# Kernel tuning notes

Measured on AMD Instinct MI355X. Metric: run time of the kernel, lower is better.

The kernel has to match this reference:

```python
import jax, jax.numpy as jnp
import numpy as np

H = 128      # hidden_dim
N = 200000   # number of available (job, machine) ops
M = 1000     # machine nodes
J = 5000     # job nodes


def setup_inputs() -> dict:
    key = jax.random.key(0)
    ks = jax.random.split(key, 8)
    s = 0.05  # weight scale
    return {
        "x_graph": jax.random.normal(ks[0], (1, 2 * H), jnp.float32),
        "x_m": jax.random.normal(ks[1], (M, H), jnp.float32),
        "x_job": jax.random.normal(ks[2], (J, H), jnp.float32),
        "m_ids": jax.random.randint(ks[3], (N,), 0, M),
        "job_idx": jax.random.randint(ks[4], (N,), 0, J),
        "W0": jax.random.normal(ks[5], (4 * H, H), jnp.float32) * s,
        "b0": jnp.zeros((H,), jnp.float32),
        "W1": jax.random.normal(ks[6], (H, H), jnp.float32) * s,
        "b1": jnp.zeros((H,), jnp.float32),
        "W2": jax.random.normal(ks[7], (H, 1), jnp.float32) * s,
        "b2": jnp.zeros((1,), jnp.float32),
    }


def reference(x_graph, x_m, x_job, m_ids, job_idx, W0, b0, W1, b1, W2, b2):
    n = m_ids.shape[0]
    # vectorized form of the python loop: [x_graph | x_m[m_id] | x_job[job_pos]] -> [N, 4H]
    feats = jnp.concatenate(
        [
            jnp.broadcast_to(x_graph, (n, x_graph.shape[1])),
            x_m[m_ids],
            x_job[job_idx],
        ],
        axis=1,
    )
    h = jax.nn.relu(feats @ W0 + b0)   # Linear(4H -> H) + ReLU
    h = jax.nn.relu(h @ W1 + b1)       # Linear(H -> H) + ReLU
    scores = (h @ W2 + b2)[:, 0]       # Linear(H -> 1), squeeze -> [N]
    logp = jax.nn.log_softmax(scores, axis=0)
    probs = jnp.exp(logp)
    idx = jnp.argmax(scores)           # greedy selection (deterministic baseline)
    entropy = -jnp.sum(probs * logp)   # Categorical entropy
    return idx, probs[idx], logp[idx], entropy
```

## Files before the change

kernel.cpp:

```cpp
#include <hip/hip_runtime.h>
#include <math.h>

#define HID 128
#define TILE_R 64
#define TILE_P 32
#define XS_STRIDE 132
#define H0S_STRIDE 136
#define DELTA 0.05f

typedef short bf16x8 __attribute__((ext_vector_type(8)));
typedef float f32x4 __attribute__((ext_vector_type(4)));

static __device__ __forceinline__ unsigned short f2bf(float f) {
    union { float f; unsigned u; } v; v.f = f;
    unsigned r = v.u + 0x7FFFu + ((v.u >> 16) & 1u);
    return (unsigned short)(r >> 16);
}
static __device__ __forceinline__ float bflo(unsigned u) {
    union { unsigned u; float f; } v; v.u = u << 16; return v.f;
}
static __device__ __forceinline__ float bfhi(unsigned u) {
    union { unsigned u; float f; } v; v.u = u & 0xFFFF0000u; return v.f;
}

#define FMA4(avc, wv)                         \
    acc[r][0] = fmaf(avc, wv.x, acc[r][0]);   \
    acc[r][1] = fmaf(avc, wv.y, acc[r][1]);   \
    acc[r][2] = fmaf(avc, wv.z, acc[r][2]);   \
    acc[r][3] = fmaf(avc, wv.w, acc[r][3]);

__global__ __launch_bounds__(256, 4) void precompute_kernel(
    const float* __restrict__ x_graph,
    const float* __restrict__ x_m,
    const float* __restrict__ x_job,
    const float* __restrict__ W0,
    const float* __restrict__ b0,
    const float* __restrict__ W1,
    float* __restrict__ g,
    unsigned short* __restrict__ Pbf,
    unsigned short* __restrict__ W1T,
    int M, int J, int aTiles, int bTiles)
{
    const int t = threadIdx.x;
    const int bid = blockIdx.x;

    if (bid == 0) {
        __shared__ float xg[2 * HID];
        if (t < HID) { xg[t] = x_graph[t]; xg[t + HID] = x_graph[t + HID]; }
        __syncthreads();
        if (t < HID) {
            float acc = b0[t];
            #pragma unroll 8
            for (int k = 0; k < 2 * HID; ++k)
                acc = fmaf(xg[k], W0[k * HID + t], acc);
            g[t] = acc;
        }
        return;
    }
    if (bid == 1 + aTiles + bTiles) {
        for (int e = t; e < HID * HID; e += 256) {
            int n = e >> 7, k = e & 127;
            W1T[e] = f2bf(W1[k * HID + n]);
        }
        return;
    }

    const int tb = bid - 1;
    const float* X;
    const float* W;
    int r0, nr, dstBase;
    if (tb < aTiles) {
        r0 = tb * TILE_P;
        nr = min(TILE_P, M - r0);
        X = x_m + (size_t)r0 * HID;
        W = W0 + 2 * HID * HID;
        dstBase = r0;
    } else {
        int jb = tb - aTiles;
        r0 = jb * TILE_P;
        nr = min(TILE_P, J - r0);
        X = x_job + (size_t)r0 * HID;
        W = W0 + 3 * HID * HID;
        dstBase = M + r0;
    }

    __shared__ float xs[TILE_P * XS_STRIDE];
    {
        int row = t >> 3;
        int e = t & 7;
        #pragma unroll
        for (int u = 0; u < 4; ++u) {
            int c = e * 16 + u * 4;
            float4 v = (row < nr) ? *(const float4*)(X + row * HID + c)
                                  : make_float4(0.f, 0.f, 0.f, 0.f);
            *(float4*)&xs[row * XS_STRIDE + c] = v;
        }
    }
    __syncthreads();

    const int w = t >> 6;
    const int l = t & 63;
    const int tc = l & 7;
    const int tr = l >> 3;
    const int c0 = w * 32 + tc * 4;

    float acc[4][4];
    #pragma unroll
    for (int r = 0; r < 4; ++r)
        #pragma unroll
        for (int c = 0; c < 4; ++c) acc[r][c] = 0.0f;

    #pragma unroll 2
    for (int k0 = 0; k0 < HID; k0 += 4) {
        float4 w0v = *(const float4*)(W + (k0 + 0) * HID + c0);
        float4 w1v = *(const float4*)(W + (k0 + 1) * HID + c0);
        float4 w2m = *(const float4*)(W + (k0 + 2) * HID + c0);
        float4 w3v = *(const float4*)(W + (k0 + 3) * HID + c0);
        #pragma unroll
        for (int r = 0; r < 4; ++r) {
            float4 a = *(const float4*)&xs[(r * 8 + tr) * XS_STRIDE + k0];
            FMA4(a.x, w0v)
            FMA4(a.y, w1v)
            FMA4(a.z, w2m)
            FMA4(a.w, w3v)
        }
    }

    #pragma unroll
    for (int r = 0; r < 4; ++r) {
        int row = r * 8 + tr;
        if (row < nr) {
            unsigned lo0 = (unsigned)f2bf(acc[r][0]) | ((unsigned)f2bf(acc[r][1]) << 16);
            unsigned lo1 = (unsigned)f2bf(acc[r][2]) | ((unsigned)f2bf(acc[r][3]) << 16);
            uint2 pk = make_uint2(lo0, lo1);
            *(uint2*)(Pbf + (size_t)(dstBase + row) * HID + c0) = pk;
        }
    }
}

__global__ __launch_bounds__(256, 3) void main_kernel(
    const int* __restrict__ m_ids,
    const int* __restrict__ job_idx,
    const float* __restrict__ b1,
    const float* __restrict__ W2,
    const float* __restrict__ b2,
    const float* __restrict__ g,
    const unsigned short* __restrict__ Pbf,
    const unsigned short* __restrict__ W1T,
    float* __restrict__ scores,
    float4* __restrict__ partials,
    int N, int M)
{
    __shared__ __align__(16) short h0s[TILE_R * H0S_STRIDE];
    __shared__ __align__(16) short w1s[HID * H0S_STRIDE];
    __shared__ float sred[TILE_R];

    const int t = threadIdx.x;
    const int row0 = blockIdx.x * TILE_R;

    {
        const uint4* src = (const uint4*)W1T;
        #pragma unroll
        for (int e = t; e < 2048; e += 256) {
            int n = e >> 4, pos = e & 15;
            *(uint4*)&w1s[n * H0S_STRIDE + pos * 8] = src[e];
        }
    }

    {
        int row = t >> 2;
        int q = t & 3;
        int grow = row0 + row;
        int gr = (grow < N) ? grow : (N - 1);
        int m = m_ids[gr];
        int j = job_idx[gr];
        const unsigned short* pm = Pbf + (size_t)m * HID + q * 32;
        const unsigned short* pj = Pbf + (size_t)(M + j) * HID + q * 32;
        const float* gp = g + q * 32;
        short* dst = &h0s[row * H0S_STRIDE + q * 32];
        #pragma unroll
        for (int u = 0; u < 4; ++u) {
            uint4 mv = *(const uint4*)(pm + u * 8);
            uint4 jv = *(const uint4*)(pj + u * 8);
            float4 g0 = *(const float4*)(gp + u * 8);
            float4 g1 = *(const float4*)(gp + u * 8 + 4);
            float h0v = fmaxf(bflo(mv.x) + bflo(jv.x) + g0.x, 0.f);
            float h1v = fmaxf(bfhi(mv.x) + bfhi(jv.x) + g0.y, 0.f);
            float h2v = fmaxf(bflo(mv.y) + bflo(jv.y) + g0.z, 0.f);
            float h3v = fmaxf(bfhi(mv.y) + bfhi(jv.y) + g0.w, 0.f);
            float h4v = fmaxf(bflo(mv.z) + bflo(jv.z) + g1.x, 0.f);
            float h5v = fmaxf(bfhi(mv.z) + bfhi(jv.z) + g1.y, 0.f);
            float h6v = fmaxf(bflo(mv.w) + bflo(jv.w) + g1.z, 0.f);
            float h7v = fmaxf(bfhi(mv.w) + bfhi(jv.w) + g1.w, 0.f);
            uint4 pk;
            pk.x = (unsigned)f2bf(h0v) | ((unsigned)f2bf(h1v) << 16);
            pk.y = (unsigned)f2bf(h2v) | ((unsigned)f2bf(h3v) << 16);
            pk.z = (unsigned)f2bf(h4v) | ((unsigned)f2bf(h5v) << 16);
            pk.w = (unsigned)f2bf(h6v) | ((unsigned)f2bf(h7v) << 16);
            *(uint4*)(dst + u * 8) = pk;
        }
    }
    __syncthreads();

    const int l = t & 63;
    const int w = t >> 6;
    const int quad = l >> 4;
    const int mrow = l & 15;

    bf16x8 af[4];
    const short* ab = &h0s[(w * 16 + mrow) * H0S_STRIDE + quad * 8];
    #pragma unroll
    for (int kc = 0; kc < 4; ++kc)
        af[kc] = *(const bf16x8*)(ab + kc * 32);

    f32x4 acc[8];
    #pragma unroll
    for (int nt = 0; nt < 8; ++nt) {
        f32x4 z = {0.f, 0.f, 0.f, 0.f};
        acc[nt] = z;
    }

    const short* bb = &w1s[mrow * H0S_STRIDE + quad * 8];
    #pragma unroll
    for (int nt = 0; nt < 8; ++nt) {
        #pragma unroll
        for (int kc = 0; kc < 4; ++kc) {
            bf16x8 bfr = *(const bf16x8*)(bb + nt * 16 * H0S_STRIDE + kc * 32);
            acc[nt] = __builtin_amdgcn_mfma_f32_16x16x32_bf16(af[kc], bfr, acc[nt], 0, 0, 0);
        }
    }

    float p0 = 0.f, p1 = 0.f, p2 = 0.f, p3 = 0.f;
    #pragma unroll
    for (int nt = 0; nt < 8; ++nt) {
        int c = nt * 16 + mrow;
        float b1v = b1[c], w2v = W2[c];
        p0 += fmaxf(acc[nt][0] + b1v, 0.f) * w2v;
        p1 += fmaxf(acc[nt][1] + b1v, 0.f) * w2v;
        p2 += fmaxf(acc[nt][2] + b1v, 0.f) * w2v;
        p3 += fmaxf(acc[nt][3] + b1v, 0.f) * w2v;
    }
    #pragma unroll
    for (int off = 1; off < 16; off <<= 1) {
        p0 += __shfl_xor(p0, off);
        p1 += __shfl_xor(p1, off);
        p2 += __shfl_xor(p2, off);
        p3 += __shfl_xor(p3, off);
    }
    if (mrow == 0) {
        int rb = w * 16 + quad * 4;
        sred[rb + 0] = p0;
        sred[rb + 1] = p1;
        sred[rb + 2] = p2;
        sred[rb + 3] = p3;
    }
    __syncthreads();

    if (t < 64) {
        int grow = row0 + t;
        float s = sred[t] + b2[0];
        if (grow < N) scores[grow] = s;
        else s = -1e30f;

        float mmax = s;
        int midx = grow;
        #pragma unroll
        for (int off = 1; off < 64; off <<= 1) {
            float om = __shfl_xor(mmax, off);
            int oi = __shfl_xor(midx, off);
            if (om > mmax || (om == mmax && oi < midx)) { mmax = om; midx = oi; }
        }
        float d = s - mmax;
        float e = expf(d);
        float z = e;
        float ss = d * e;
        #pragma unroll
        for (int off = 1; off < 64; off <<= 1) {
            z += __shfl_xor(z, off);
            ss += __shfl_xor(ss, off);
        }
        if (t == 0)
            partials[blockIdx.x] = make_float4(mmax, z, ss, (float)midx);
    }
}

__device__ inline void sm_merge(float& am, float& az, float& ass, int& ai,
                                float bm, float bz, float bss, int bi)
{
    if (bm > am || (bm == am && bi < ai)) {
        float tm = am, tz = az, ts = ass; int ti = ai;
        am = bm; az = bz; ass = bss; ai = bi;
        bm = tm; bz = tz; bss = ts; bi = ti;
    }
    float f = expf(bm - am);
    az += bz * f;
    ass += (bss + (bm - am) * bz) * f;
}

__global__ __launch_bounds__(256) void scan_kernel(
    const float4* __restrict__ partials, int nparts,
    const float* __restrict__ scores,
    const int* __restrict__ m_ids,
    const int* __restrict__ job_idx,
    const float* __restrict__ x_m,
    const float* __restrict__ x_job,
    const float* __restrict__ W0,
    const float* __restrict__ W1,
    const float* __restrict__ b1,
    const float* __restrict__ W2,
    const float* __restrict__ b2,
    const float* __restrict__ g,
    float2* __restrict__ bests,
    int N)
{
    __shared__ int cand[256];
    __shared__ int ccount;
    __shared__ float rs[4];
    __shared__ int ri[4];
    __shared__ float mmx[4];

    const int t = threadIdx.x;
    const int w = t >> 6;
    const int l = t & 63;
    const int base = blockIdx.x * 256;

    float mhat = -1e30f;
    for (int i = t; i < nparts; i += 256)
        mhat = fmaxf(mhat, partials[i].x);
    #pragma unroll
    for (int off = 1; off < 64; off <<= 1)
        mhat = fmaxf(mhat, __shfl_xor(mhat, off));
    if (l == 0) mmx[w] = mhat;
    if (t == 0) ccount = 0;
    __syncthreads();
    mhat = fmaxf(fmaxf(mmx[0], mmx[1]), fmaxf(mmx[2], mmx[3]));
    const float cut = mhat - DELTA;

    int i = base + t;
    if (i < N && scores[i] >= cut) {
        int p = atomicAdd(&ccount, 1);
        cand[p] = i;
    }
    __syncthreads();
    const int nc = ccount;
    if (nc == 0) {
        if (t == 0) bests[blockIdx.x] = make_float2(-1e30f, __int_as_float(0x7fffffff));
        return;
    }

    float bs = -1e30f;
    int bi = 0x7fffffff;
    for (int c = w; c < nc; c += 4) {
        int gr = cand[c];
        int mm = m_ids[gr];
        int jj = job_idx[gr];
        const float* xm = x_m + (size_t)mm * HID;
        const float* xj = x_job + (size_t)jj * HID;
        const float* wm = W0 + 2 * HID * HID;
        const float* wj = W0 + 3 * HID * HID;
        float a0 = g[l], a1 = g[l + 64];
        for (int k = 0; k < HID; ++k) {
            float xmk = xm[k];
            float xjk = xj[k];
            a0 = fmaf(xmk, wm[k * HID + l], a0);
            a1 = fmaf(xmk, wm[k * HID + l + 64], a1);
            a0 = fmaf(xjk, wj[k * HID + l], a0);
            a1 = fmaf(xjk, wj[k * HID + l + 64], a1);
        }
        a0 = fmaxf(a0, 0.f);
        a1 = fmaxf(a1, 0.f);
        float acc0 = 0.f, acc1 = 0.f;
        for (int k = 0; k < 64; ++k) {
            float h = __shfl(a0, k);
            acc0 = fmaf(h, W1[k * HID + l], acc0);
            acc1 = fmaf(h, W1[k * HID + l + 64], acc1);
        }
        for (int k = 0; k < 64; ++k) {
            float h = __shfl(a1, k);
            acc0 = fmaf(h, W1[(k + 64) * HID + l], acc0);
            acc1 = fmaf(h, W1[(k + 64) * HID + l + 64], acc1);
        }
        float p = fmaxf(acc0 + b1[l], 0.f) * W2[l]
                + fmaxf(acc1 + b1[l + 64], 0.f) * W2[l + 64];
        #pragma unroll
        for (int off = 1; off < 64; off <<= 1)
            p += __shfl_xor(p, off);
        float s = p + b2[0];
        if (s > bs || (s == bs && gr < bi)) { bs = s; bi = gr; }
    }
    if (l == 0) { rs[w] = bs; ri[w] = bi; }
    __syncthreads();
    if (t == 0) {
        float best = rs[0];
        int bwin = ri[0];
        for (int i2 = 1; i2 < 4; ++i2)
            if (rs[i2] > best || (rs[i2] == best && ri[i2] < bwin)) {
                best = rs[i2]; bwin = ri[i2];
            }
        bests[blockIdx.x] = make_float2(best, __int_as_float(bwin));
    }
}

__global__ __launch_bounds__(256) void finalize_kernel(
    const float4* __restrict__ partials, int nparts,
    const float2* __restrict__ bests, int nblocks,
    float* __restrict__ out)
{
    __shared__ float4 wred[4];
    __shared__ int widx[4];
    __shared__ float rs[4];
    __shared__ int ri[4];
    const int t = threadIdx.x;
    const int w = t >> 6;
    const int l = t & 63;

    float m = -1e30f, z = 0.f, ss = 0.f;
    int idx = 0x7fffffff;
    for (int i = t; i < nparts; i += 256) {
        float4 p = partials[i];
        sm_merge(m, z, ss, idx, p.x, p.y, p.z, (int)p.w);
    }
    #pragma unroll
    for (int off = 1; off < 64; off <<= 1) {
        float om = __shfl_xor(m, off);
        float oz = __shfl_xor(z, off);
        float os = __shfl_xor(ss, off);
        int oi = __shfl_xor(idx, off);
        sm_merge(m, z, ss, idx, om, oz, os, oi);
    }
    if (l == 0) { wred[w] = make_float4(m, z, ss, 0.f); widx[w] = idx; }

    float bs = -1e30f;
    int bi = 0x7fffffff;
    for (int i = t; i < nblocks; i += 256) {
        float2 b = bests[i];
        int gi = __float_as_int(b.y);
        if (b.x > bs || (b.x == bs && gi < bi)) { bs = b.x; bi = gi; }
    }
    #pragma unroll
    for (int off = 1; off < 64; off <<= 1) {
        float os = __shfl_xor(bs, off);
        int oi = __shfl_xor(bi, off);
        if (os > bs || (os == bs && oi < bi)) { bs = os; bi = oi; }
    }
    if (l == 0) { rs[w] = bs; ri[w] = bi; }
    __syncthreads();

    if (t == 0) {
        for (int i = 1; i < 4; ++i) {
            sm_merge(m, z, ss, idx, wred[i].x, wred[i].y, wred[i].z, widx[i]);
            if (rs[i] > bs || (rs[i] == bs && ri[i] < bi)) { bs = rs[i]; bi = ri[i]; }
        }
        float logZ = logf(z);
        out[0] = (float)bi;
        out[1] = expf(bs - m) / z;
        out[2] = (bs - m) - logZ;
        out[3] = logZ - ss / z;
    }
}

extern "C" void kernel_launch(void* const* d_in, const int* in_sizes, int n_in,
                              void* d_out, int out_size, void* d_ws, size_t ws_size,
                              hipStream_t stream)
{
    const float* x_graph = (const float*)d_in[0];
    const float* x_m     = (const float*)d_in[1];
    const float* x_job   = (const float*)d_in[2];
    const int*   m_ids   = (const int*)d_in[3];
    const int*   job_idx = (const int*)d_in[4];
    const float* W0      = (const float*)d_in[5];
    const float* b0      = (const float*)d_in[6];
    const float* W1      = (const float*)d_in[7];
    const float* b1      = (const float*)d_in[8];
    const float* W2      = (const float*)d_in[9];
    const float* b2      = (const float*)d_in[10];
    float* out = (float*)d_out;

    const int N = in_sizes[3];
    const int M = in_sizes[1] / HID;
    const int J = in_sizes[2] / HID;

    const int tiles = (N + TILE_R - 1) / TILE_R;
    const int aTiles = (M + TILE_P - 1) / TILE_P;
    const int bTiles = (J + TILE_P - 1) / TILE_P;
    const int sblocks = (N + 255) / 256;

    float* ws = (float*)d_ws;
    float* g = ws;
    float* scores = ws + HID;
    float4* partials = (float4*)(scores + N);
    float2* bests = (float2*)(partials + tiles);
    unsigned short* W1T = (unsigned short*)(bests + sblocks + (sblocks & 1));
    unsigned short* Pbf = W1T + HID * HID;

    precompute_kernel<<<1 + aTiles + bTiles + 1, 256, 0, stream>>>(
        x_graph, x_m, x_job, W0, b0, W1, g, Pbf, W1T, M, J, aTiles, bTiles);
    main_kernel<<<tiles, 256, 0, stream>>>(
        m_ids, job_idx, b1, W2, b2, g, Pbf, W1T, scores, partials, N, M);
    scan_kernel<<<sblocks, 256, 0, stream>>>(
        partials, tiles, scores, m_ids, job_idx, x_m, x_job, W0, W1, b1, W2, b2,
        g, bests, N);
    finalize_kernel<<<1, 256, 0, stream>>>(partials, tiles, bests, sblocks, out);
}
```

Baseline: 145.0 us.

## Make main kernel persistent to amortize W1 shared-memory load; compact tile maxima

Changes the main kernel from one block per 64-row tile to a fixed grid of blocks that loop over tiles. Each block now loads W1 into shared memory once instead of once per tile. Each tile also writes its maximum to a compact float array, so the scan kernel reads a dense array with four independent accumulators instead of strided float4 partials. This cuts redundant W1 loads and scan-side bandwidth. In exchange, the gather load of each tile no longer overlaps with other blocks' compute as freely, and the fixed grid of 1042 blocks may not balance evenly across the ~3125 tiles.

```diff
diff --git a/kernel.cpp b/kernel.cpp
--- a/kernel.cpp
+++ b/kernel.cpp
@@ -7,6 +7,7 @@
 #define XS_STRIDE 132
 #define H0S_STRIDE 136
 #define DELTA 0.05f
+#define MAIN_GRID 1042
 
 typedef short bf16x8 __attribute__((ext_vector_type(8)));
 typedef float f32x4 __attribute__((ext_vector_type(4)));
@@ -149,138 +150,143 @@
     const unsigned short* __restrict__ W1T,
     float* __restrict__ scores,
     float4* __restrict__ partials,
-    int N, int M)
+    float* __restrict__ tmax,
+    int N, int M, int tiles)
 {
     __shared__ __align__(16) short h0s[TILE_R * H0S_STRIDE];
     __shared__ __align__(16) short w1s[HID * H0S_STRIDE];
     __shared__ float sred[TILE_R];
 
     const int t = threadIdx.x;
-    const int row0 = blockIdx.x * TILE_R;
-
-    {
-        const uint4* src = (const uint4*)W1T;
-        #pragma unroll
-        for (int e = t; e < 2048; e += 256) {
-            int n = e >> 4, pos = e & 15;
-            *(uint4*)&w1s[n * H0S_STRIDE + pos * 8] = src[e];
-        }
-    }
-
-    {
-        int row = t >> 2;
-        int q = t & 3;
-        int grow = row0 + row;
-        int gr = (grow < N) ? grow : (N - 1);
-        int m = m_ids[gr];
-        int j = job_idx[gr];
-        const unsigned short* pm = Pbf + (size_t)m * HID + q * 32;
-        const unsigned short* pj = Pbf + (size_t)(M + j) * HID + q * 32;
-        const float* gp = g + q * 32;
-        short* dst = &h0s[row * H0S_STRIDE + q * 32];
-        #pragma unroll
-        for (int u = 0; u < 4; ++u) {
-            uint4 mv = *(const uint4*)(pm + u * 8);
-            uint4 jv = *(const uint4*)(pj + u * 8);
-            float4 g0 = *(const float4*)(gp + u * 8);
-            float4 g1 = *(const float4*)(gp + u * 8 + 4);
-            float h0v = fmaxf(bflo(mv.x) + bflo(jv.x) + g0.x, 0.f);
-            float h1v = fmaxf(bfhi(mv.x) + bfhi(jv.x) + g0.y, 0.f);
-            float h2v = fmaxf(bflo(mv.y) + bflo(jv.y) + g0.z, 0.f);
-            float h3v = fmaxf(bfhi(mv.y) + bfhi(jv.y) + g0.w, 0.f);
-            float h4v = fmaxf(bflo(mv.z) + bflo(jv.z) + g1.x, 0.f);
-            float h5v = fmaxf(bfhi(mv.z) + bfhi(jv.z) + g1.y, 0.f);
-            float h6v = fmaxf(bflo(mv.w) + bflo(jv.w) + g1.z, 0.f);
-            float h7v = fmaxf(bfhi(mv.w) + bfhi(jv.w) + g1.w, 0.f);
-            uint4 pk;
-            pk.x = (unsigned)f2bf(h0v) | ((unsigned)f2bf(h1v) << 16);
-            pk.y = (unsigned)f2bf(h2v) | ((unsigned)f2bf(h3v) << 16);
-            pk.z = (unsigned)f2bf(h4v) | ((unsigned)f2bf(h5v) << 16);
-            pk.w = (unsigned)f2bf(h6v) | ((unsigned)f2bf(h7v) << 16);
-            *(uint4*)(dst + u * 8) = pk;
-        }
-    }
-    __syncthreads();
-
     const int l = t & 63;
     const int w = t >> 6;
     const int quad = l >> 4;
     const int mrow = l & 15;
 
-    bf16x8 af[4];
-    const short* ab = &h0s[(w * 16 + mrow) * H0S_STRIDE + quad * 8];
-    #pragma unroll
-    for (int kc = 0; kc < 4; ++kc)
-        af[kc] = *(const bf16x8*)(ab + kc * 32);
-
-    f32x4 acc[8];
-    #pragma unroll
-    for (int nt = 0; nt < 8; ++nt) {
-        f32x4 z = {0.f, 0.f, 0.f, 0.f};
-        acc[nt] = z;
-    }
-
-    const short* bb = &w1s[mrow * H0S_STRIDE + quad * 8];
-    #pragma unroll
-    for (int nt = 0; nt < 8; ++nt) {
-        #pragma unroll
-        for (int kc = 0; kc < 4; ++kc) {
-            bf16x8 bfr = *(const bf16x8*)(bb + nt * 16 * H0S_STRIDE + kc * 32);
-            acc[nt] = __builtin_amdgcn_mfma_f32_16x16x32_bf16(af[kc], bfr, acc[nt], 0, 0, 0);
-        }
-    }
-
-    float p0 = 0.f, p1 = 0.f, p2 = 0.f, p3 = 0.f;
-    #pragma unroll
-    for (int nt = 0; nt < 8; ++nt) {
-        int c = nt * 16 + mrow;
-        float b1v = b1[c], w2v = W2[c];
-        p0 += fmaxf(acc[nt][0] + b1v, 0.f) * w2v;
-        p1 += fmaxf(acc[nt][1] + b1v, 0.f) * w2v;
-        p2 += fmaxf(acc[nt][2] + b1v, 0.f) * w2v;
-        p3 += fmaxf(acc[nt][3] + b1v, 0.f) * w2v;
-    }
-    #pragma unroll
-    for (int off = 1; off < 16; off <<= 1) {
-        p0 += __shfl_xor(p0, off);
-        p1 += __shfl_xor(p1, off);
-        p2 += __shfl_xor(p2, off);
-        p3 += __shfl_xor(p3, off);
-    }
-    if (mrow == 0) {
-        int rb = w * 16 + quad * 4;
-        sred[rb + 0] = p0;
-        sred[rb + 1] = p1;
-        sred[rb + 2] = p2;
-        sred[rb + 3] = p3;
-    }
-    __syncthreads();
-
-    if (t < 64) {
-        int grow = row0 + t;
-        float s = sred[t] + b2[0];
-        if (grow < N) scores[grow] = s;
-        else s = -1e30f;
-
-        float mmax = s;
-        int midx = grow;
-        #pragma unroll
-        for (int off = 1; off < 64; off <<= 1) {
-            float om = __shfl_xor(mmax, off);
-            int oi = __shfl_xor(midx, off);
-            if (om > mmax || (om == mmax && oi < midx)) { mmax = om; midx = oi; }
-        }
-        float d = s - mmax;
-        float e = expf(d);
-        float z = e;
-        float ss = d * e;
-        #pragma unroll
-        for (int off = 1; off < 64; off <<= 1) {
-            z += __shfl_xor(z, off);
-            ss += __shfl_xor(ss, off);
-        }
-        if (t == 0)
-            partials[blockIdx.x] = make_float4(mmax, z, ss, (float)midx);
+    {
+        const uint4* src = (const uint4*)W1T;
+        #pragma unroll
+        for (int e = t; e < 2048; e += 256) {
+            int n = e >> 4, pos = e & 15;
+            *(uint4*)&w1s[n * H0S_STRIDE + pos * 8] = src[e];
+        }
+    }
+
+    for (int tile = blockIdx.x; tile < tiles; tile += MAIN_GRID) {
+        const int row0 = tile * TILE_R;
+
+        {
+            int row = t >> 2;
+            int q = t & 3;
+            int grow = row0 + row;
+            int gr = (grow < N) ? grow : (N - 1);
+            int m = m_ids[gr];
+            int j = job_idx[gr];
+            const unsigned short* pm = Pbf + (size_t)m * HID + q * 32;
+            const unsigned short* pj = Pbf + (size_t)(M + j) * HID + q * 32;
+            const float* gp = g + q * 32;
+            short* dst = &h0s[row * H0S_STRIDE + q * 32];
+            #pragma unroll
+            for (int u = 0; u < 4; ++u) {
+                uint4 mv = *(const uint4*)(pm + u * 8);
+                uint4 jv = *(const uint4*)(pj + u * 8);
+                float4 g0 = *(const float4*)(gp + u * 8);
+                float4 g1 = *(const float4*)(gp + u * 8 + 4);
+                float h0v = fmaxf(bflo(mv.x) + bflo(jv.x) + g0.x, 0.f);
+                float h1v = fmaxf(bfhi(mv.x) + bfhi(jv.x) + g0.y, 0.f);
+                float h2v = fmaxf(bflo(mv.y) + bflo(jv.y) + g0.z, 0.f);
+                float h3v = fmaxf(bfhi(mv.y) + bfhi(jv.y) + g0.w, 0.f);
+                float h4v = fmaxf(bflo(mv.z) + bflo(jv.z) + g1.x, 0.f);
+                float h5v = fmaxf(bfhi(mv.z) + bfhi(jv.z) + g1.y, 0.f);
+                float h6v = fmaxf(bflo(mv.w) + bflo(jv.w) + g1.z, 0.f);
+                float h7v = fmaxf(bfhi(mv.w) + bfhi(jv.w) + g1.w, 0.f);
+                uint4 pk;
+                pk.x = (unsigned)f2bf(h0v) | ((unsigned)f2bf(h1v) << 16);
+                pk.y = (unsigned)f2bf(h2v) | ((unsigned)f2bf(h3v) << 16);
+                pk.z = (unsigned)f2bf(h4v) | ((unsigned)f2bf(h5v) << 16);
+                pk.w = (unsigned)f2bf(h6v) | ((unsigned)f2bf(h7v) << 16);
+                *(uint4*)(dst + u * 8) = pk;
+            }
+        }
+        __syncthreads();
+
+        bf16x8 af[4];
+        const short* ab = &h0s[(w * 16 + mrow) * H0S_STRIDE + quad * 8];
+        #pragma unroll
+        for (int kc = 0; kc < 4; ++kc)
+            af[kc] = *(const bf16x8*)(ab + kc * 32);
+
+        f32x4 acc[8];
+        #pragma unroll
+        for (int nt = 0; nt < 8; ++nt) {
+            f32x4 z = {0.f, 0.f, 0.f, 0.f};
+            acc[nt] = z;
+        }
+
+        const short* bb = &w1s[mrow * H0S_STRIDE + quad * 8];
+        #pragma unroll
+        for (int nt = 0; nt < 8; ++nt) {
+            #pragma unroll
+            for (int kc = 0; kc < 4; ++kc) {
+                bf16x8 bfr = *(const bf16x8*)(bb + nt * 16 * H0S_STRIDE + kc * 32);
+                acc[nt] = __builtin_amdgcn_mfma_f32_16x16x32_bf16(af[kc], bfr, acc[nt], 0, 0, 0);
+            }
+        }
+
+        float p0 = 0.f, p1 = 0.f, p2 = 0.f, p3 = 0.f;
+        #pragma unroll
+        for (int nt = 0; nt < 8; ++nt) {
+            int c = nt * 16 + mrow;
+            float b1v = b1[c], w2v = W2[c];
+            p0 += fmaxf(acc[nt][0] + b1v, 0.f) * w2v;
+            p1 += fmaxf(acc[nt][1] + b1v, 0.f) * w2v;
+            p2 += fmaxf(acc[nt][2] + b1v, 0.f) * w2v;
+            p3 += fmaxf(acc[nt][3] + b1v, 0.f) * w2v;
+        }
+        #pragma unroll
+        for (int off = 1; off < 16; off <<= 1) {
+            p0 += __shfl_xor(p0, off);
+            p1 += __shfl_xor(p1, off);
+            p2 += __shfl_xor(p2, off);
+            p3 += __shfl_xor(p3, off);
+        }
+        if (mrow == 0) {
+            int rb = w * 16 + quad * 4;
+            sred[rb + 0] = p0;
+            sred[rb + 1] = p1;
+            sred[rb + 2] = p2;
+            sred[rb + 3] = p3;
+        }
+        __syncthreads();
+
+        if (t < 64) {
+            int grow = row0 + t;
+            float s = sred[t] + b2[0];
+            if (grow < N) scores[grow] = s;
+            else s = -1e30f;
+
+            float mmax = s;
+            int midx = grow;
+            #pragma unroll
+            for (int off = 1; off < 64; off <<= 1) {
+                float om = __shfl_xor(mmax, off);
+                int oi = __shfl_xor(midx, off);
+                if (om > mmax || (om == mmax && oi < midx)) { mmax = om; midx = oi; }
+            }
+            float d = s - mmax;
+            float e = expf(d);
+            float z = e;
+            float ss = d * e;
+            #pragma unroll
+            for (int off = 1; off < 64; off <<= 1) {
+                z += __shfl_xor(z, off);
+                ss += __shfl_xor(ss, off);
+            }
+            if (t == 0) {
+                partials[tile] = make_float4(mmax, z, ss, (float)midx);
+                tmax[tile] = mmax;
+            }
+        }
     }
 }
 
@@ -298,7 +304,7 @@
 }
 
 __global__ __launch_bounds__(256) void scan_kernel(
-    const float4* __restrict__ partials, int nparts,
+    const float* __restrict__ tmax, int nparts,
     const float* __restrict__ scores,
     const int* __restrict__ m_ids,
     const int* __restrict__ job_idx,
@@ -324,9 +330,16 @@
     const int l = t & 63;
     const int base = blockIdx.x * 256;
 
-    float mhat = -1e30f;
-    for (int i = t; i < nparts; i += 256)
-        mhat = fmaxf(mhat, partials[i].x);
+    float m0 = -1e30f, m1 = -1e30f, m2 = -1e30f, m3 = -1e30f;
+    int i = t;
+    for (; i + 768 < nparts; i += 1024) {
+        m0 = fmaxf(m0, tmax[i]);
+        m1 = fmaxf(m1, tmax[i + 256]);
+        m2 = fmaxf(m2, tmax[i + 512]);
+        m3 = fmaxf(m3, tmax[i + 768]);
+    }
+    for (; i < nparts; i += 256) m0 = fmaxf(m0, tmax[i]);
+    float mhat = fmaxf(fmaxf(m0, m1), fmaxf(m2, m3));
     #pragma unroll
     for (int off = 1; off < 64; off <<= 1)
         mhat = fmaxf(mhat, __shfl_xor(mhat, off));
@@ -336,10 +349,10 @@
     mhat = fmaxf(fmaxf(mmx[0], mmx[1]), fmaxf(mmx[2], mmx[3]));
     const float cut = mhat - DELTA;
 
-    int i = base + t;
-    if (i < N && scores[i] >= cut) {
+    int idx = base + t;
+    if (idx < N && scores[idx] >= cut) {
         int p = atomicAdd(&ccount, 1);
-        cand[p] = i;
+        cand[p] = idx;
     }
     __syncthreads();
     const int nc = ccount;
@@ -489,16 +502,19 @@
     float* g = ws;
     float* scores = ws + HID;
     float4* partials = (float4*)(scores + N);
-    float2* bests = (float2*)(partials + tiles);
+    float* tmax = (float*)(partials + tiles);
+    const int tmaxPad = (tiles + 3) & ~3;
+    float2* bests = (float2*)(tmax + tmaxPad);
     unsigned short* W1T = (unsigned short*)(bests + sblocks + (sblocks & 1));
     unsigned short* Pbf = W1T + HID * HID;
 
     precompute_kernel<<<1 + aTiles + bTiles + 1, 256, 0, stream>>>(
         x_graph, x_m, x_job, W0, b0, W1, g, Pbf, W1T, M, J, aTiles, bTiles);
-    main_kernel<<<tiles, 256, 0, stream>>>(
-        m_ids, job_idx, b1, W2, b2, g, Pbf, W1T, scores, partials, N, M);
+    main_kernel<<<MAIN_GRID, 256, 0, stream>>>(
+        m_ids, job_idx, b1, W2, b2, g, Pbf, W1T, scores, partials, tmax,
+        N, M, tiles);
     scan_kernel<<<sblocks, 256, 0, stream>>>(
-        partials, tiles, scores, m_ids, job_idx, x_m, x_job, W0, W1, b1, W2, b2,
+        tmax, tiles, scores, m_ids, job_idx, x_m, x_job, W0, W1, b1, W2, b2,
         g, bests, N);
     finalize_kernel<<<1, 256, 0, stream>>>(partials, tiles, bests, sblocks, out);
 }
```

Measured after the change: 141.1 us. 2.7% less time.
